# Kernel optimization log

Measured on AMD Instinct MI355X. Metric: run time of the kernel, lower is better.

Reference implementation:

```python
import jax, jax.numpy as jnp
import numpy as np

B, T, D, H = 2, 4096, 768, 12
HD = D // H  # head_dim = 64


def setup_inputs() -> dict:
    key = jax.random.key(0)
    ks = jax.random.split(key, 6)
    s = 0.02
    return {
        "x": jax.random.normal(ks[0], (B, T, D), dtype=jnp.float32),
        "Wq": jax.random.normal(ks[1], (D, D), dtype=jnp.float32) * s,
        "Wk": jax.random.normal(ks[2], (D, D), dtype=jnp.float32) * s,
        "Wv": jax.random.normal(ks[3], (D, D), dtype=jnp.float32) * s,
        "Wo": jax.random.normal(ks[4], (D, D), dtype=jnp.float32) * s,
        "bo": jnp.zeros((D,), dtype=jnp.float32),
    }


def reference(x, Wq, Wk, Wv, Wo, bo):
    b, t, d = x.shape
    # QKV projections (no bias), reshape to [B, H, T, HD]
    def heads(w):
        return (x @ w.T).reshape(b, t, H, HD).transpose(0, 2, 1, 3)
    q, k, v = heads(Wq), heads(Wk), heads(Wv)
    scores = jnp.einsum("bhqd,bhkd->bhqk", q, k)  # [B,H,T,T]
    causal = jnp.tril(jnp.ones((t, t), dtype=bool))
    scores = jnp.where(causal, scores, -jnp.inf)
    attn = jax.nn.softmax(scores / jnp.sqrt(jnp.float32(HD)), axis=-1)
    ctx = jnp.einsum("bhqk,bhkd->bhqd", attn, v)  # [B,H,T,HD]
    ctx = ctx.transpose(0, 2, 1, 3).reshape(b, t, d)
    return ctx @ Wo.T + bo
```

## Files before the change

kernel.cpp:

```cpp
#include <hip/hip_runtime.h>
#include <hip/hip_bf16.h>
#include <cstdint>
#include <cstddef>

#define B_  2
#define T_  4096
#define D_  768
#define H_  12
#define HD_ 64
#define M_  (B_*T_)

#define SCL 0.18033688f

typedef __bf16 bf16x8 __attribute__((ext_vector_type(8)));
typedef float  f32x4  __attribute__((ext_vector_type(4)));
using bf16 = __hip_bfloat16;

__device__ inline float fexp2(float x) {
  float r; asm("v_exp_f32 %0, %1" : "=v"(r) : "v"(x)); return r;
}
__device__ inline uint32_t fu(float x) { union { float f; uint32_t u; } c; c.f = x; return c.u; }
__device__ inline uint32_t pktr(float a, float b) {
  return __builtin_amdgcn_perm(fu(b), fu(a), 0x07060302);
}
#define GLD16(g, l) __builtin_amdgcn_global_load_lds( \
    (const __attribute__((address_space(1))) uint32_t*)(const void*)(g), \
    (__attribute__((address_space(3))) uint32_t*)(void*)(l), 16, 0, 0)

__global__ void cvt_all(const float* __restrict__ x,
                        const float* __restrict__ w0, const float* __restrict__ w1,
                        const float* __restrict__ w2, const float* __restrict__ w3,
                        bf16* __restrict__ xd,
                        bf16* __restrict__ d0, bf16* __restrict__ d1,
                        bf16* __restrict__ d2, bf16* __restrict__ d3) {
  int blk = blockIdx.x;
  const float* s; bf16* d; int i;
  if (blk < 6144) {
    s = x; d = xd; i = blk * 256 + threadIdx.x;
  } else {
    int q = blk - 6144, which = q / 576, rb = q % 576;
    switch (which) {
      case 0: s = w0; d = d0; break;
      case 1: s = w1; d = d1; break;
      case 2: s = w2; d = d2; break;
      default: s = w3; d = d3; break;
    }
    i = rb * 256 + threadIdx.x;
  }
  float4 v = ((const float4*)s)[i];
  union { bf16 o[4]; uint2 u; } pk;
  pk.o[0] = __float2bfloat16(v.x); pk.o[1] = __float2bfloat16(v.y);
  pk.o[2] = __float2bfloat16(v.z); pk.o[3] = __float2bfloat16(v.w);
  *(uint2*)(d + 4 * (size_t)i) = pk.u;
}

__global__ __launch_bounds__(256) void gemm_qkv(const bf16* __restrict__ x,
                                                const bf16* __restrict__ W0,
                                                const bf16* __restrict__ W1,
                                                const bf16* __restrict__ W2,
                                                bf16* __restrict__ O0,
                                                bf16* __restrict__ O1,
                                                bf16* __restrict__ O2t) {
  __shared__ bf16 As[2][4096];
  __shared__ bf16 Bs[2][4096];
  const int flat = blockIdx.x;
  const int by = flat / 18;
  const int rr = flat % 18;
  const int z  = rr / 6;
  const int bx = rr % 6;
  const bf16* Wz = (z == 0) ? W0 : ((z == 1) ? W1 : W2);
  const char* Ap; const char* Bp; int a0, b0;
  if (z == 2) { Ap = (const char*)x;  a0 = by * 128; Bp = (const char*)Wz; b0 = bx * 128; }
  else        { Ap = (const char*)Wz; a0 = bx * 128; Bp = (const char*)x;  b0 = by * 128; }
  const int t = threadIdx.x;
  const int w = t >> 6, lane = t & 63;
  const int wa = (w >> 1) * 64, wb = (w & 1) * 64;
  const int mi = lane & 15, qd = lane >> 4;

  int aoff[2], boff[2];
  #pragma unroll
  for (int i = 0; i < 2; ++i) {
    int L = i * 256 + t;
    int row = L >> 2, sl = L & 3, c = sl ^ (row & 3);
    aoff[i] = (a0 + row) * 1536 + c * 16;
    boff[i] = (b0 + row) * 1536 + c * 16;
  }
  const int fsw = (qd ^ (mi & 3)) * 8;

  f32x4 acc[4][4] = {};

  #pragma unroll
  for (int i = 0; i < 2; ++i) {
    GLD16(Ap + aoff[i], &As[0][i * 2048 + w * 512]);
    GLD16(Bp + boff[i], &Bs[0][i * 2048 + w * 512]);
  }

  for (int kk = 0; kk < 24; ++kk) {
    __syncthreads();
    const int par = kk & 1;
    if (kk + 1 < 24) {
      const int np = par ^ 1, kb = (kk + 1) * 64;
      #pragma unroll
      for (int i = 0; i < 2; ++i) {
        GLD16(Ap + aoff[i] + kb, &As[np][i * 2048 + w * 512]);
        GLD16(Bp + boff[i] + kb, &Bs[np][i * 2048 + w * 512]);
      }
    }
    bf16x8 af[4], bfr[4];
    #pragma unroll
    for (int at = 0; at < 4; ++at)
      af[at] = *(const bf16x8*)&As[par][(wa + at * 16 + mi) * 32 + fsw];
    #pragma unroll
    for (int bt = 0; bt < 4; ++bt)
      bfr[bt] = *(const bf16x8*)&Bs[par][(wb + bt * 16 + mi) * 32 + fsw];
    #pragma unroll
    for (int at = 0; at < 4; ++at)
      #pragma unroll
      for (int bt = 0; bt < 4; ++bt)
        acc[at][bt] = __builtin_amdgcn_mfma_f32_16x16x32_bf16(af[at], bfr[bt], acc[at][bt], 0, 0, 0);
  }

  if (z == 2) {
    #pragma unroll
    for (int at = 0; at < 4; ++at)
      #pragma unroll
      for (int bt = 0; bt < 4; ++bt) {
        int gr = a0 + wa + at * 16 + qd * 4;
        int gc = b0 + wb + bt * 16 + mi;
        union { bf16 o[4]; uint2 u; } pk;
        #pragma unroll
        for (int r = 0; r < 4; ++r) pk.o[r] = __float2bfloat16(acc[at][bt][r]);
        int bb = gr >> 12, tt = gr & 4095;
        *(uint2*)(O2t + (size_t)bb * 768 * 4096 + (size_t)gc * 4096 + tt) = pk.u;
      }
  } else {
    const float scl = (z == 1) ? SCL : 1.0f;
    bf16* Ob = (z == 0) ? O0 : O1;
    #pragma unroll
    for (int at = 0; at < 4; ++at)
      #pragma unroll
      for (int bt = 0; bt < 4; ++bt) {
        int f0  = a0 + wa + at * 16 + qd * 4;
        int tkn = b0 + wb + bt * 16 + mi;
        union { bf16 o[4]; uint2 u; } pk;
        #pragma unroll
        for (int r = 0; r < 4; ++r) pk.o[r] = __float2bfloat16(acc[at][bt][r] * scl);
        *(uint2*)(Ob + (size_t)tkn * 768 + f0) = pk.u;
      }
  }
}

__global__ __launch_bounds__(256) void gemm_out(const bf16* __restrict__ ctx,
                                                const bf16* __restrict__ Wo,
                                                float* __restrict__ Cf,
                                                const float* __restrict__ bias) {
  __shared__ bf16 As[2][2048];
  __shared__ bf16 Bs[2][4096];
  const int flat = blockIdx.x;
  const int by = flat / 12, bx = flat % 12;
  const char* Ap = (const char*)Wo;  const int a0 = bx * 64;
  const char* Bp = (const char*)ctx; const int b0 = by * 128;
  const int t = threadIdx.x;
  const int w = t >> 6, lane = t & 63;
  const int wa = (w >> 1) * 32, wb = (w & 1) * 64;
  const int mi = lane & 15, qd = lane >> 4;

  int aoff, boff[2];
  { int row = t >> 2, sl = t & 3, c = sl ^ (row & 3);
    aoff = (a0 + row) * 1536 + c * 16; }
  #pragma unroll
  for (int i = 0; i < 2; ++i) {
    int L = i * 256 + t;
    int row = L >> 2, sl = L & 3, c = sl ^ (row & 3);
    boff[i] = (b0 + row) * 1536 + c * 16;
  }
  const int fsw = (qd ^ (mi & 3)) * 8;

  f32x4 acc[2][4] = {};

  GLD16(Ap + aoff, &As[0][w * 512]);
  #pragma unroll
  for (int i = 0; i < 2; ++i)
    GLD16(Bp + boff[i], &Bs[0][i * 2048 + w * 512]);

  for (int kk = 0; kk < 24; ++kk) {
    __syncthreads();
    const int par = kk & 1;
    if (kk + 1 < 24) {
      const int np = par ^ 1, kb = (kk + 1) * 64;
      GLD16(Ap + aoff + kb, &As[np][w * 512]);
      #pragma unroll
      for (int i = 0; i < 2; ++i)
        GLD16(Bp + boff[i] + kb, &Bs[np][i * 2048 + w * 512]);
    }
    bf16x8 af[2], bfr[4];
    #pragma unroll
    for (int at = 0; at < 2; ++at)
      af[at] = *(const bf16x8*)&As[par][(wa + at * 16 + mi) * 32 + fsw];
    #pragma unroll
    for (int bt = 0; bt < 4; ++bt)
      bfr[bt] = *(const bf16x8*)&Bs[par][(wb + bt * 16 + mi) * 32 + fsw];
    #pragma unroll
    for (int at = 0; at < 2; ++at)
      #pragma unroll
      for (int bt = 0; bt < 4; ++bt)
        acc[at][bt] = __builtin_amdgcn_mfma_f32_16x16x32_bf16(af[at], bfr[bt], acc[at][bt], 0, 0, 0);
  }

  #pragma unroll
  for (int at = 0; at < 2; ++at)
    #pragma unroll
    for (int bt = 0; bt < 4; ++bt) {
      int f0  = a0 + wa + at * 16 + qd * 4;
      int tkn = b0 + wb + bt * 16 + mi;
      float4 bv = *(const float4*)&bias[f0];
      float4 o;
      o.x = acc[at][bt][0] + bv.x; o.y = acc[at][bt][1] + bv.y;
      o.z = acc[at][bt][2] + bv.z; o.w = acc[at][bt][3] + bv.w;
      *(float4*)&Cf[(size_t)tkn * 768 + f0] = o;
    }
}

__global__ __launch_bounds__(128, 2) void flash_attn(const bf16* __restrict__ Q,
                                                     const bf16* __restrict__ K,
                                                     const bf16* __restrict__ Vt,
                                                     bf16* __restrict__ ctx) {
  __shared__ bf16 Ks[2][4096];
  __shared__ bf16 Vs[2][4096];
  const int t = threadIdx.x;
  const int w = t >> 6, lane = t & 63;
  const int mi = lane & 15, qd = lane >> 4;
  const int bh   = blockIdx.x % 24;
  const int qrev = blockIdx.x / 24;
  const int q0 = T_ - 64 - qrev * 64;
  const int b = bh / H_, h = bh % H_;
  const size_t bTD = (size_t)b * T_ * D_;
  const char* Kp = (const char*)(K  + bTD + (size_t)h * HD_);
  const char* Vp = (const char*)(Vt + (size_t)b * D_ * T_ + (size_t)h * HD_ * T_);
  const int qw = q0 + w * 32;

  int vkoff[4], vvoff[4];
  #pragma unroll
  for (int i = 0; i < 4; ++i) {
    int L = i * 128 + t;
    int rl = L >> 3, c = (L & 7) ^ (rl & 7);
    int jrow = (rl & 32) | ((rl & 0xC) << 1) | ((rl & 16) >> 2) | (rl & 3);
    vkoff[i] = jrow * 1536 + c * 16;
    vvoff[i] = rl * 8192 + c * 16;
  }

  int fidx[4][2];
  #pragma unroll
  for (int jt = 0; jt < 4; ++jt)
    #pragma unroll
    for (int kt = 0; kt < 2; ++kt)
      fidx[jt][kt] = (jt * 16 + mi) * 64 + (((kt * 4 + qd) ^ (mi & 7)) * 8);

  bf16x8 qf[2][2];
  const bf16* Qp = Q + bTD + (size_t)h * HD_;
  #pragma unroll
  for (int s = 0; s < 2; ++s)
    #pragma unroll
    for (int kt = 0; kt < 2; ++kt)
      qf[s][kt] = *(const bf16x8*)(Qp + (size_t)(qw + s * 16 + mi) * D_ + kt * 32 + qd * 8);

  f32x4 oacc[2][4] = {};
  float lst[2] = {0.f, 0.f};
  const int ntiles = q0 / 64 + 1;

  #pragma unroll
  for (int i = 0; i < 4; ++i) {
    GLD16(Kp + vkoff[i], &Ks[0][i * 1024 + w * 512]);
    GLD16(Vp + vvoff[i], &Vs[0][i * 1024 + w * 512]);
  }

  for (int tt = 0; tt < ntiles; ++tt) {
    __syncthreads();
    const int par = tt & 1;
    if (tt + 1 < ntiles) {
      const size_t j1 = (size_t)(tt + 1) * 64;
      const int np = par ^ 1;
      #pragma unroll
      for (int i = 0; i < 4; ++i) {
        GLD16(Kp + vkoff[i] + j1 * 1536, &Ks[np][i * 1024 + w * 512]);
        GLD16(Vp + vvoff[i] + j1 * 2,    &Vs[np][i * 1024 + w * 512]);
      }
    }
    const int j0 = tt * 64;

    f32x4 sacc[2][4] = {};
    __builtin_amdgcn_s_setprio(1);
    #pragma unroll
    for (int jt = 0; jt < 4; ++jt)
      #pragma unroll
      for (int kt = 0; kt < 2; ++kt) {
        bf16x8 kf = *(const bf16x8*)&Ks[par][fidx[jt][kt]];
        sacc[0][jt] = __builtin_amdgcn_mfma_f32_16x16x32_bf16(kf, qf[0][kt], sacc[0][jt], 0, 0, 0);
        sacc[1][jt] = __builtin_amdgcn_mfma_f32_16x16x32_bf16(kf, qf[1][kt], sacc[1][jt], 0, 0, 0);
      }
    __builtin_amdgcn_s_setprio(0);

    if (j0 + 63 > qw) {
      #pragma unroll
      for (int s = 0; s < 2; ++s) {
        const int qg = qw + s * 16 + mi;
        #pragma unroll
        for (int jt = 0; jt < 4; ++jt)
          #pragma unroll
          for (int r = 0; r < 4; ++r) {
            int jg = j0 + ((jt >> 1) << 5) + (qd << 3) + ((jt & 1) << 2) + r;
            if (jg > qg) sacc[s][jt][r] = -1e30f;
          }
      }
    }

    bf16x8 pB[2][2];
    #pragma unroll
    for (int s = 0; s < 2; ++s) {
      uint32_t pu[4][2];
      #pragma unroll
      for (int jt = 0; jt < 4; ++jt) {
        float p0 = fexp2(sacc[s][jt][0]);
        float p1 = fexp2(sacc[s][jt][1]);
        float p2 = fexp2(sacc[s][jt][2]);
        float p3 = fexp2(sacc[s][jt][3]);
        lst[s] += (p0 + p1) + (p2 + p3);
        pu[jt][0] = pktr(p0, p1);
        pu[jt][1] = pktr(p2, p3);
      }
      #pragma unroll
      for (int kt = 0; kt < 2; ++kt) {
        union { uint32_t u[4]; bf16x8 v; } m;
        m.u[0] = pu[2 * kt][0];     m.u[1] = pu[2 * kt][1];
        m.u[2] = pu[2 * kt + 1][0]; m.u[3] = pu[2 * kt + 1][1];
        pB[s][kt] = m.v;
      }
    }

    __builtin_amdgcn_s_setprio(1);
    #pragma unroll
    for (int kt = 0; kt < 2; ++kt)
      #pragma unroll
      for (int dt = 0; dt < 4; ++dt) {
        bf16x8 vf = *(const bf16x8*)&Vs[par][fidx[dt][kt]];
        oacc[0][dt] = __builtin_amdgcn_mfma_f32_16x16x32_bf16(vf, pB[0][kt], oacc[0][dt], 0, 0, 0);
        oacc[1][dt] = __builtin_amdgcn_mfma_f32_16x16x32_bf16(vf, pB[1][kt], oacc[1][dt], 0, 0, 0);
      }
    __builtin_amdgcn_s_setprio(0);
  }

  #pragma unroll
  for (int s = 0; s < 2; ++s) {
    float l = lst[s];
    l += __shfl_xor(l, 16);
    l += __shfl_xor(l, 32);
    float inv = __builtin_amdgcn_rcpf(l);
    const int qg = qw + s * 16 + mi;
    bf16* cp = ctx + bTD + (size_t)qg * D_ + h * HD_ + qd * 4;
    #pragma unroll
    for (int dt = 0; dt < 4; ++dt) {
      union { bf16 o[4]; uint2 u; } pko;
      #pragma unroll
      for (int r = 0; r < 4; ++r) pko.o[r] = __float2bfloat16(oacc[s][dt][r] * inv);
      *(uint2*)(cp + dt * 16) = pko.u;
    }
  }
}

extern "C" void kernel_launch(void* const* d_in, const int* in_sizes, int n_in,
                              void* d_out, int out_size, void* d_ws, size_t ws_size,
                              hipStream_t stream) {
  const float* x  = (const float*)d_in[0];
  const float* Wq = (const float*)d_in[1];
  const float* Wk = (const float*)d_in[2];
  const float* Wv = (const float*)d_in[3];
  const float* Wo = (const float*)d_in[4];
  const float* bo = (const float*)d_in[5];
  float* out = (float*)d_out;

  char* ws = (char*)d_ws;
  const size_t SZ  = (size_t)M_ * D_ * 2;
  const size_t WSZ = (size_t)D_ * D_ * 2;
  bf16* xb   = (bf16*)(ws);
  bf16* Qb   = (bf16*)(ws + 1 * SZ);
  bf16* Kb   = (bf16*)(ws + 2 * SZ);
  bf16* Vtg  = (bf16*)(ws + 3 * SZ);
  bf16* ctxb = (bf16*)(ws + 4 * SZ);
  bf16* Wqb  = (bf16*)(ws + 5 * SZ);
  bf16* Wkb  = (bf16*)(ws + 5 * SZ + 1 * WSZ);
  bf16* Wvb  = (bf16*)(ws + 5 * SZ + 2 * WSZ);
  bf16* Wob  = (bf16*)(ws + 5 * SZ + 3 * WSZ);

  cvt_all<<<6144 + 4 * 576, 256, 0, stream>>>(x, Wq, Wk, Wv, Wo, xb, Wqb, Wkb, Wvb, Wob);

  gemm_qkv<<<1152, 256, 0, stream>>>(xb, Wqb, Wkb, Wvb, Qb, Kb, Vtg);

  flash_attn<<<(T_ / 64) * B_ * H_, 128, 0, stream>>>(Qb, Kb, Vtg, ctxb);

  gemm_out<<<768, 256, 0, stream>>>(ctxb, Wob, out, bo);
}
```

Baseline: 247.6 us.

## Split flash attention KV tile across four waves with split-K reduction

The attention block grows from 2 to 4 waves. Each wave now handles one 32-query half and one 32-key half of every 64-key tile, and the two key-half partial outputs and row sums are combined through shared memory at the end. Waves whose key half lies fully above the causal diagonal skip the tile's compute. This raises per-block parallelism and occupancy and trims masked work, at the cost of an extra LDS reduction, more barriers, and a tighter register budget under the new launch bounds.

```diff
diff --git a/kernel.cpp b/kernel.cpp
--- a/kernel.cpp
+++ b/kernel.cpp
@@ -221,7 +221,7 @@
     }
 }
 
-__global__ __launch_bounds__(128, 2) void flash_attn(const bf16* __restrict__ Q,
+__global__ __launch_bounds__(256, 5) void flash_attn(const bf16* __restrict__ Q,
                                                      const bf16* __restrict__ K,
                                                      const bf16* __restrict__ Vt,
                                                      bf16* __restrict__ ctx) {
@@ -230,6 +230,7 @@
   const int t = threadIdx.x;
   const int w = t >> 6, lane = t & 63;
   const int mi = lane & 15, qd = lane >> 4;
+  const int qhalf = w >> 1, jhalf = w & 1;
   const int bh   = blockIdx.x % 24;
   const int qrev = blockIdx.x / 24;
   const int q0 = T_ - 64 - qrev * 64;
@@ -237,24 +238,29 @@
   const size_t bTD = (size_t)b * T_ * D_;
   const char* Kp = (const char*)(K  + bTD + (size_t)h * HD_);
   const char* Vp = (const char*)(Vt + (size_t)b * D_ * T_ + (size_t)h * HD_ * T_);
-  const int qw = q0 + w * 32;
-
-  int vkoff[4], vvoff[4];
-  #pragma unroll
-  for (int i = 0; i < 4; ++i) {
-    int L = i * 128 + t;
+  const int qw = q0 + qhalf * 32;
+  const int jb = jhalf * 32;
+
+  int vkoff[2], vvoff[2];
+  #pragma unroll
+  for (int i = 0; i < 2; ++i) {
+    int L = i * 256 + t;
     int rl = L >> 3, c = (L & 7) ^ (rl & 7);
     int jrow = (rl & 32) | ((rl & 0xC) << 1) | ((rl & 16) >> 2) | (rl & 3);
     vkoff[i] = jrow * 1536 + c * 16;
     vvoff[i] = rl * 8192 + c * 16;
   }
 
-  int fidx[4][2];
-  #pragma unroll
-  for (int jt = 0; jt < 4; ++jt)
+  int fidxk[2][2];
+  #pragma unroll
+  for (int jl = 0; jl < 2; ++jl)
     #pragma unroll
     for (int kt = 0; kt < 2; ++kt)
-      fidx[jt][kt] = (jt * 16 + mi) * 64 + (((kt * 4 + qd) ^ (mi & 7)) * 8);
+      fidxk[jl][kt] = ((2 * jhalf + jl) * 16 + mi) * 64 + (((kt * 4 + qd) ^ (mi & 7)) * 8);
+  int fidxv[4];
+  #pragma unroll
+  for (int dt = 0; dt < 4; ++dt)
+    fidxv[dt] = (dt * 16 + mi) * 64 + (((jhalf * 4 + qd) ^ (mi & 7)) * 8);
 
   bf16x8 qf[2][2];
   const bf16* Qp = Q + bTD + (size_t)h * HD_;
@@ -269,9 +275,9 @@
   const int ntiles = q0 / 64 + 1;
 
   #pragma unroll
-  for (int i = 0; i < 4; ++i) {
-    GLD16(Kp + vkoff[i], &Ks[0][i * 1024 + w * 512]);
-    GLD16(Vp + vvoff[i], &Vs[0][i * 1024 + w * 512]);
+  for (int i = 0; i < 2; ++i) {
+    GLD16(Kp + vkoff[i], &Ks[0][i * 2048 + w * 512]);
+    GLD16(Vp + vvoff[i], &Vs[0][i * 2048 + w * 512]);
   }
 
   for (int tt = 0; tt < ntiles; ++tt) {
@@ -281,88 +287,106 @@
       const size_t j1 = (size_t)(tt + 1) * 64;
       const int np = par ^ 1;
       #pragma unroll
-      for (int i = 0; i < 4; ++i) {
-        GLD16(Kp + vkoff[i] + j1 * 1536, &Ks[np][i * 1024 + w * 512]);
-        GLD16(Vp + vvoff[i] + j1 * 2,    &Vs[np][i * 1024 + w * 512]);
+      for (int i = 0; i < 2; ++i) {
+        GLD16(Kp + vkoff[i] + j1 * 1536, &Ks[np][i * 2048 + w * 512]);
+        GLD16(Vp + vvoff[i] + j1 * 2,    &Vs[np][i * 2048 + w * 512]);
       }
     }
     const int j0 = tt * 64;
-
-    f32x4 sacc[2][4] = {};
+    if (j0 + jb > qw + 31) continue;
+
+    f32x4 sacc[2][2] = {};
     __builtin_amdgcn_s_setprio(1);
     #pragma unroll
-    for (int jt = 0; jt < 4; ++jt)
+    for (int jl = 0; jl < 2; ++jl)
       #pragma unroll
       for (int kt = 0; kt < 2; ++kt) {
-        bf16x8 kf = *(const bf16x8*)&Ks[par][fidx[jt][kt]];
-        sacc[0][jt] = __builtin_amdgcn_mfma_f32_16x16x32_bf16(kf, qf[0][kt], sacc[0][jt], 0, 0, 0);
-        sacc[1][jt] = __builtin_amdgcn_mfma_f32_16x16x32_bf16(kf, qf[1][kt], sacc[1][jt], 0, 0, 0);
+        bf16x8 kf = *(const bf16x8*)&Ks[par][fidxk[jl][kt]];
+        sacc[0][jl] = __builtin_amdgcn_mfma_f32_16x16x32_bf16(kf, qf[0][kt], sacc[0][jl], 0, 0, 0);
+        sacc[1][jl] = __builtin_amdgcn_mfma_f32_16x16x32_bf16(kf, qf[1][kt], sacc[1][jl], 0, 0, 0);
       }
     __builtin_amdgcn_s_setprio(0);
 
-    if (j0 + 63 > qw) {
+    if (j0 + jb + 31 > qw) {
       #pragma unroll
       for (int s = 0; s < 2; ++s) {
         const int qg = qw + s * 16 + mi;
         #pragma unroll
-        for (int jt = 0; jt < 4; ++jt)
+        for (int jl = 0; jl < 2; ++jl)
           #pragma unroll
           for (int r = 0; r < 4; ++r) {
-            int jg = j0 + ((jt >> 1) << 5) + (qd << 3) + ((jt & 1) << 2) + r;
-            if (jg > qg) sacc[s][jt][r] = -1e30f;
+            int jg = j0 + jb + (qd << 3) + (jl << 2) + r;
+            if (jg > qg) sacc[s][jl][r] = -1e30f;
           }
       }
     }
 
-    bf16x8 pB[2][2];
+    bf16x8 pB[2];
     #pragma unroll
     for (int s = 0; s < 2; ++s) {
-      uint32_t pu[4][2];
-      #pragma unroll
-      for (int jt = 0; jt < 4; ++jt) {
-        float p0 = fexp2(sacc[s][jt][0]);
-        float p1 = fexp2(sacc[s][jt][1]);
-        float p2 = fexp2(sacc[s][jt][2]);
-        float p3 = fexp2(sacc[s][jt][3]);
+      uint32_t pu[2][2];
+      #pragma unroll
+      for (int jl = 0; jl < 2; ++jl) {
+        float p0 = fexp2(sacc[s][jl][0]);
+        float p1 = fexp2(sacc[s][jl][1]);
+        float p2 = fexp2(sacc[s][jl][2]);
+        float p3 = fexp2(sacc[s][jl][3]);
         lst[s] += (p0 + p1) + (p2 + p3);
-        pu[jt][0] = pktr(p0, p1);
-        pu[jt][1] = pktr(p2, p3);
-      }
-      #pragma unroll
-      for (int kt = 0; kt < 2; ++kt) {
-        union { uint32_t u[4]; bf16x8 v; } m;
-        m.u[0] = pu[2 * kt][0];     m.u[1] = pu[2 * kt][1];
-        m.u[2] = pu[2 * kt + 1][0]; m.u[3] = pu[2 * kt + 1][1];
-        pB[s][kt] = m.v;
-      }
+        pu[jl][0] = pktr(p0, p1);
+        pu[jl][1] = pktr(p2, p3);
+      }
+      union { uint32_t u[4]; bf16x8 v; } m;
+      m.u[0] = pu[0][0]; m.u[1] = pu[0][1];
+      m.u[2] = pu[1][0]; m.u[3] = pu[1][1];
+      pB[s] = m.v;
     }
 
     __builtin_amdgcn_s_setprio(1);
     #pragma unroll
-    for (int kt = 0; kt < 2; ++kt)
+    for (int dt = 0; dt < 4; ++dt) {
+      bf16x8 vf = *(const bf16x8*)&Vs[par][fidxv[dt]];
+      oacc[0][dt] = __builtin_amdgcn_mfma_f32_16x16x32_bf16(vf, pB[0], oacc[0][dt], 0, 0, 0);
+      oacc[1][dt] = __builtin_amdgcn_mfma_f32_16x16x32_bf16(vf, pB[1], oacc[1][dt], 0, 0, 0);
+    }
+    __builtin_amdgcn_s_setprio(0);
+  }
+
+  __syncthreads();
+  float* red  = (float*)&Ks[0][0];
+  float* lred = (float*)&Vs[0][0];
+  if (jhalf == 1) {
+    #pragma unroll
+    for (int s = 0; s < 2; ++s)
+      #pragma unroll
+      for (int dt = 0; dt < 4; ++dt)
+        *(f32x4*)&red[qhalf * 2048 + (s * 4 + dt) * 256 + lane * 4] = oacc[s][dt];
+    *(float2*)&lred[qhalf * 128 + lane * 2] = make_float2(lst[0], lst[1]);
+  }
+  __syncthreads();
+  if (jhalf == 0) {
+    float2 lp = *(const float2*)&lred[qhalf * 128 + lane * 2];
+    lst[0] += lp.x; lst[1] += lp.y;
+    #pragma unroll
+    for (int s = 0; s < 2; ++s) {
       #pragma unroll
       for (int dt = 0; dt < 4; ++dt) {
-        bf16x8 vf = *(const bf16x8*)&Vs[par][fidx[dt][kt]];
-        oacc[0][dt] = __builtin_amdgcn_mfma_f32_16x16x32_bf16(vf, pB[0][kt], oacc[0][dt], 0, 0, 0);
-        oacc[1][dt] = __builtin_amdgcn_mfma_f32_16x16x32_bf16(vf, pB[1][kt], oacc[1][dt], 0, 0, 0);
-      }
-    __builtin_amdgcn_s_setprio(0);
-  }
-
-  #pragma unroll
-  for (int s = 0; s < 2; ++s) {
-    float l = lst[s];
-    l += __shfl_xor(l, 16);
-    l += __shfl_xor(l, 32);
-    float inv = __builtin_amdgcn_rcpf(l);
-    const int qg = qw + s * 16 + mi;
-    bf16* cp = ctx + bTD + (size_t)qg * D_ + h * HD_ + qd * 4;
-    #pragma unroll
-    for (int dt = 0; dt < 4; ++dt) {
-      union { bf16 o[4]; uint2 u; } pko;
-      #pragma unroll
-      for (int r = 0; r < 4; ++r) pko.o[r] = __float2bfloat16(oacc[s][dt][r] * inv);
-      *(uint2*)(cp + dt * 16) = pko.u;
+        f32x4 o2 = *(const f32x4*)&red[qhalf * 2048 + (s * 4 + dt) * 256 + lane * 4];
+        oacc[s][dt][0] += o2[0]; oacc[s][dt][1] += o2[1];
+        oacc[s][dt][2] += o2[2]; oacc[s][dt][3] += o2[3];
+      }
+      float l = lst[s];
+      l += __shfl_xor(l, 16);
+      l += __shfl_xor(l, 32);
+      float inv = __builtin_amdgcn_rcpf(l);
+      const int qg = qw + s * 16 + mi;
+      bf16* cp = ctx + bTD + (size_t)qg * D_ + h * HD_ + qd * 4;
+      #pragma unroll
+      for (int dt = 0; dt < 4; ++dt) {
+        union { bf16 o[4]; uint2 u; } pko;
+        #pragma unroll
+        for (int r = 0; r < 4; ++r) pko.o[r] = __float2bfloat16(oacc[s][dt][r] * inv);
+        *(uint2*)(cp + dt * 16) = pko.u;
+      }
     }
   }
 }
@@ -395,7 +419,7 @@
 
   gemm_qkv<<<1152, 256, 0, stream>>>(xb, Wqb, Wkb, Wvb, Qb, Kb, Vtg);
 
-  flash_attn<<<(T_ / 64) * B_ * H_, 128, 0, stream>>>(Qb, Kb, Vtg, ctxb);
+  flash_attn<<<(T_ / 64) * B_ * H_, 256, 0, stream>>>(Qb, Kb, Vtg, ctxb);
 
   gemm_out<<<768, 256, 0, stream>>>(ctxb, Wob, out, bo);
 }
```

After: 237.4 us. -4.1%, faster.
